# Kernel optimization log

Hardware: AMD Instinct MI355X
Metric: run time of the kernel (lower is better)

Reference implementation:

```python
import jax, jax.numpy as jnp
import numpy as np

DEPTH = 4
CODEBOOK_NUM = 2048
CODEBOOK_DIM = 256


def setup_inputs() -> dict:
    key = jax.random.key(0)
    k1, k2 = jax.random.split(key)
    z = jax.random.normal(k1, (32, CODEBOOK_DIM, 32, 32), dtype=jnp.float32)
    # matches nn.init.uniform_(weight, -1/K, 1/K)
    codebook = jax.random.uniform(
        k2, (CODEBOOK_NUM, CODEBOOK_DIM), dtype=jnp.float32,
        minval=-1.0 / CODEBOOK_NUM, maxval=1.0 / CODEBOOK_NUM)
    return {"z": z, "codebook": codebook}


def _quantize(flat_z, codebook):
    # ||z||^2 + ||e||^2 - 2 z.e  -> [N, K]
    dists = (jnp.sum(flat_z ** 2, axis=1, keepdims=True)
             + jnp.sum(codebook ** 2, axis=1)
             - 2.0 * flat_z @ codebook.T)
    indices = jnp.argmin(dists, axis=1)          # [N]
    return codebook[indices], indices            # gather [N, C]


def reference(z, codebook):
    B, C, H, W = z.shape
    K = codebook.shape[0]
    residual = z
    q_list, idx_list = [], []
    for _ in range(DEPTH):
        flat = residual.transpose(0, 2, 3, 1).reshape(-1, C)   # [N, C]
        q_flat, idx = _quantize(flat, codebook)
        q = q_flat.reshape(B, H, W, C).transpose(0, 3, 1, 2)   # [B, C, H, W]
        q_list.append(q)
        idx_list.append(idx)
        residual = residual - q
    # prefix-sum across depth (matches the in-place accumulation loop)
    quantized_cum = jnp.cumsum(jnp.stack(q_list, axis=0), axis=0)  # [D,B,C,H,W]
    q_last = quantized_cum[-1]
    # note: residual here is z_orig - sum_q, so ST term is z_orig - 2*sum_q (faithful)
    quantized_z_st = q_last + jax.lax.stop_gradient(residual - q_last)
    all_idx = jnp.concatenate(idx_list, axis=0)                    # [D*N]
    # mean of one-hot == normalized histogram (avoids [D*N, K] materialization)
    counts = jnp.zeros((K,), dtype=jnp.float32).at[all_idx].add(1.0)
    probs = counts / all_idx.shape[0]
    perplexity = jnp.exp(-jnp.sum(probs * jnp.log(jnp.clip(probs, 1e-10))))
    indices = jnp.stack(idx_list, axis=0)                          # [D, N]
    return quantized_cum, quantized_z_st, indices, perplexity
```

## Files before the change

kernel.cpp:

```cpp
#include <hip/hip_runtime.h>
#include <math.h>

#define BB 32
#define CC 256
#define HWt 1024
#define NN 32768
#define KK 2048
#define RQDEPTH 4
#define CAP 64
#define DELTA 4e-3f

typedef __attribute__((ext_vector_type(8))) short short8;
typedef __attribute__((ext_vector_type(16))) float f32x16;

__device__ __forceinline__ float pw128sq(const float4* __restrict__ a4) {
  float r[8];
  {
    float4 p = a4[0], q = a4[1];
    r[0] = __fmul_rn(p.x, p.x); r[1] = __fmul_rn(p.y, p.y);
    r[2] = __fmul_rn(p.z, p.z); r[3] = __fmul_rn(p.w, p.w);
    r[4] = __fmul_rn(q.x, q.x); r[5] = __fmul_rn(q.y, q.y);
    r[6] = __fmul_rn(q.z, q.z); r[7] = __fmul_rn(q.w, q.w);
  }
  for (int i = 1; i < 16; ++i) {
    float4 p = a4[2 * i], q = a4[2 * i + 1];
    r[0] = __fadd_rn(r[0], __fmul_rn(p.x, p.x));
    r[1] = __fadd_rn(r[1], __fmul_rn(p.y, p.y));
    r[2] = __fadd_rn(r[2], __fmul_rn(p.z, p.z));
    r[3] = __fadd_rn(r[3], __fmul_rn(p.w, p.w));
    r[4] = __fadd_rn(r[4], __fmul_rn(q.x, q.x));
    r[5] = __fadd_rn(r[5], __fmul_rn(q.y, q.y));
    r[6] = __fadd_rn(r[6], __fmul_rn(q.z, q.z));
    r[7] = __fadd_rn(r[7], __fmul_rn(q.w, q.w));
  }
  return __fadd_rn(__fadd_rn(__fadd_rn(r[0], r[1]), __fadd_rn(r[2], r[3])),
                   __fadd_rn(__fadd_rn(r[4], r[5]), __fadd_rn(r[6], r[7])));
}

__device__ __forceinline__ unsigned short f2bf(float x) {
  unsigned u = __float_as_uint(x);
  return (unsigned short)((u + 0x7fffu + ((u >> 16) & 1u)) >> 16);
}
__device__ __forceinline__ unsigned fenc(float f) {
  unsigned u = __float_as_uint(f);
  return (u & 0x80000000u) ? ~u : (u | 0x80000000u);
}
__device__ __forceinline__ float fdec(unsigned k) {
  return __uint_as_float((k & 0x80000000u) ? (k ^ 0x80000000u) : ~k);
}

__device__ __forceinline__ float exact_dot(const float4* __restrict__ zr4,
                                           const float4* __restrict__ e4) {
  float a = 0.f;
#pragma unroll 8
  for (int c4 = 0; c4 < 64; ++c4) {
    const float4 z4 = zr4[c4];
    const float4 q4 = e4[c4];
    a = fmaf(z4.x, q4.x, a);
    a = fmaf(z4.y, q4.y, a);
    a = fmaf(z4.z, q4.z, a);
    a = fmaf(z4.w, q4.w, a);
  }
  return a;
}

__global__ void k_ztrans(const float* __restrict__ z, float* __restrict__ resid) {
  __shared__ float tile[32][33];
  int b = blockIdx.z, c0 = blockIdx.y * 32, hw0 = blockIdx.x * 32;
  int tx = threadIdx.x & 31, ty = threadIdx.x >> 5;
  for (int i = ty; i < 32; i += 8)
    tile[i][tx] = z[((size_t)b * CC + c0 + i) * HWt + hw0 + tx];
  __syncthreads();
  for (int i = ty; i < 32; i += 8)
    resid[((size_t)b * HWt + hw0 + i) * CC + c0 + tx] = tile[tx][i];
}

__global__ void k_esplitH(const float* __restrict__ cb, short8* __restrict__ esH8) {
  const int tg = blockIdx.x * 256 + threadIdx.x;
  const int k = tg >> 5, c8 = tg & 31;
  const int idx8 = ((k >> 5) * 32 + c8) * 32 + (k & 31);
  const float4* s4 = (const float4*)(cb + (size_t)k * CC + c8 * 8);
  float4 p = s4[0], q = s4[1];
  short8 H;
  H[0] = (short)f2bf(p.x); H[1] = (short)f2bf(p.y);
  H[2] = (short)f2bf(p.z); H[3] = (short)f2bf(p.w);
  H[4] = (short)f2bf(q.x); H[5] = (short)f2bf(q.y);
  H[6] = (short)f2bf(q.z); H[7] = (short)f2bf(q.w);
  esH8[idx8] = H;
}

__global__ void k_bnorm(const float* __restrict__ cb, float* __restrict__ Bcol) {
  int k = blockIdx.x * 256 + threadIdx.x;
  if (k >= KK) return;
  const float4* row = (const float4*)(cb + (size_t)k * CC);
  Bcol[k] = __fadd_rn(pw128sq(row), pw128sq(row + 32));
}

__global__ void k_anorm(const float* __restrict__ resid, float* __restrict__ Arow) {
  int n = blockIdx.x * 256 + threadIdx.x;
  if (n >= NN) return;
  const float4* row = (const float4*)(resid + (size_t)n * CC);
  Arow[n] = __fadd_rn(pw128sq(row), pw128sq(row + 32));
}

__global__ void k_zero(int* counts) {
  int t = blockIdx.x * 256 + threadIdx.x;
  if (t < KK) counts[t] = 0;
}

__global__ __launch_bounds__(512, 4) void k_bulk(
    const float* __restrict__ resid, const short8* __restrict__ esH8,
    const float* __restrict__ cb, const float* __restrict__ Arow,
    const float* __restrict__ Bcol, int* __restrict__ idxAll,
    float* __restrict__ idxOut, int* __restrict__ counts, int depth) {
  __shared__ short8 zH8[32 * 32];
  __shared__ int cnt[32];
  __shared__ unsigned minkey[32];
  __shared__ unsigned long long best[32];
  __shared__ int clist[32 * CAP];

  const int t = threadIdx.x;
  const int row0 = blockIdx.x * 32;

  if (t < 32) { cnt[t] = 0; minkey[t] = 0xFFFFFFFFu; best[t] = ~0ull; }

  {
    const int srow = t & 31;
    const int c8a = (t >> 5) * 2;
#pragma unroll
    for (int cc = 0; cc < 2; ++cc) {
      const int c8 = c8a + cc;
      const float4* s4 =
          (const float4*)(resid + (size_t)(row0 + srow) * CC + c8 * 8);
      float4 p = s4[0], q = s4[1];
      short8 H;
      H[0] = (short)f2bf(p.x); H[1] = (short)f2bf(p.y);
      H[2] = (short)f2bf(p.z); H[3] = (short)f2bf(p.w);
      H[4] = (short)f2bf(q.x); H[5] = (short)f2bf(q.y);
      H[6] = (short)f2bf(q.z); H[7] = (short)f2bf(q.w);
      zH8[c8 * 32 + srow] = H;
    }
  }
  __syncthreads();

  const int wave = t >> 6, lane = t & 63;
  const int l31 = lane & 31, hh = lane >> 5;

  short8 zr[16];
  {
    const short8* zb = zH8 + hh * 32 + l31;
#pragma unroll
    for (int s = 0; s < 16; ++s) zr[s] = zb[s * 64];
  }

#pragma unroll 1
  for (int it = 0; it < 8; ++it) {
    const int kt = wave * 8 + ((it + (int)blockIdx.x) & 7);
    const int kb = kt * 32;
    f32x16 a0;
#pragma unroll
    for (int i = 0; i < 16; ++i) a0[i] = 0.f;

    const short8* ep = esH8 + kt * 1024 + hh * 32 + l31;
#pragma unroll
    for (int half = 0; half < 2; ++half) {
      short8 e[8];
#pragma unroll
      for (int s = 0; s < 8; ++s) e[s] = ep[(half * 8 + s) * 64];
#pragma unroll
      for (int s = 0; s < 8; ++s)
        a0 = __builtin_amdgcn_mfma_f32_32x32x16_bf16(zr[half * 8 + s], e[s],
                                                     a0, 0, 0, 0);
    }

    const float bkv = Bcol[kb + l31];
    float dt[16];
#pragma unroll
    for (int r = 0; r < 16; ++r) {
      const float m = a0[r];
      dt[r] = __fsub_rn(bkv, __fadd_rn(m, m));
    }
    if (it == 0) {
#pragma unroll
      for (int r = 0; r < 16; ++r) {
        float rm = dt[r];
#pragma unroll
        for (int m = 1; m < 32; m <<= 1) rm = fminf(rm, __shfl_xor(rm, m));
        if (l31 == 0) {
          const int rowr = (r & 3) + 8 * (r >> 2) + 4 * hh;
          atomicMin(&minkey[rowr], fenc(rm));
        }
      }
    }
#pragma unroll
    for (int r = 0; r < 16; ++r) {
      const int rowr = (r & 3) + 8 * (r >> 2) + 4 * hh;
      const float thr = fdec(minkey[rowr]) + DELTA;
      if (dt[r] <= thr) {
        atomicMin(&minkey[rowr], fenc(dt[r]));
        int idx = atomicAdd(&cnt[rowr], 1);
        if (idx < CAP) clist[rowr * CAP + idx] = kb + l31;
      }
    }
  }
  __syncthreads();

  {
    const int row = t >> 4;
    const int nc0 = cnt[row];
    const float av = Arow[row0 + row];
    const float4* zr4 = (const float4*)(resid + (size_t)(row0 + row) * CC);
    if (nc0 <= CAP) {
      for (int s = (t & 15); s < nc0; s += 16) {
        const int k = clist[row * CAP + s];
        const float a = exact_dot(zr4, (const float4*)(cb + (size_t)k * CC));
        const float Cv = __fadd_rn(av, Bcol[k]);
        const float sv = __fsub_rn(Cv, __fadd_rn(a, a));
        unsigned long long pk =
            ((unsigned long long)__float_as_uint(sv) << 32) | (unsigned)k;
        atomicMin(&best[row], pk);
      }
    } else {
      for (int k = (t & 15); k < KK; k += 16) {
        const float a = exact_dot(zr4, (const float4*)(cb + (size_t)k * CC));
        const float Cv = __fadd_rn(av, Bcol[k]);
        const float sv = __fsub_rn(Cv, __fadd_rn(a, a));
        unsigned long long pk =
            ((unsigned long long)__float_as_uint(sv) << 32) | (unsigned)k;
        atomicMin(&best[row], pk);
      }
    }
  }
  __syncthreads();
  if (t < 32) {
    const int wi = (int)(unsigned)(best[t] & 0xffffffffu);
    const int n = row0 + t;
    idxAll[depth * NN + n] = wi;
    idxOut[n] = (float)wi;
    atomicAdd(counts + wi, 1);
  }
}

__global__ void k_update(const float* __restrict__ cb, const int* __restrict__ idxAll,
                         float* __restrict__ resid, float* __restrict__ cum,
                         float* __restrict__ zst, int depth) {
  __shared__ float qt[32][33];
  __shared__ float rt[32][33];
  int b = blockIdx.z, c0 = blockIdx.y * 32, hw0 = blockIdx.x * 32;
  int tx = threadIdx.x & 31, ty = threadIdx.x >> 5;
  const int* idx = idxAll + depth * NN;
  for (int i = ty; i < 32; i += 8) {
    int n = b * HWt + hw0 + i;
    int kk = idx[n];
    size_t fo = (size_t)n * CC + c0 + tx;
    float q = cb[(size_t)kk * CC + c0 + tx];
    float r = __fsub_rn(resid[fo], q);
    resid[fo] = r;
    qt[i][tx] = q;
    rt[i][tx] = r;
  }
  __syncthreads();
  const size_t PLANE = (size_t)NN * CC;
  for (int i = ty; i < 32; i += 8) {
    size_t oo = ((size_t)b * CC + c0 + i) * HWt + hw0 + tx;
    float q = qt[tx][i];
    float prevv = (depth == 0) ? 0.f : cum[(size_t)(depth - 1) * PLANE + oo];
    cum[(size_t)depth * PLANE + oo] = __fadd_rn(prevv, q);
    if (depth == 3) zst[oo] = rt[tx][i];
  }
}

__global__ void k_perp(const int* __restrict__ counts, float* __restrict__ out) {
  __shared__ double sh[256];
  double s = 0.0;
  for (int k = threadIdx.x; k < KK; k += 256) {
    int c = counts[k];
    if (c > 0) {
      double p = (double)c / (double)(RQDEPTH * NN);
      s += p * log(p);
    }
  }
  sh[threadIdx.x] = s;
  __syncthreads();
  for (int st = 128; st; st >>= 1) {
    if (threadIdx.x < st) sh[threadIdx.x] += sh[threadIdx.x + st];
    __syncthreads();
  }
  if (threadIdx.x == 0) out[0] = (float)exp(-sh[0]);
}

extern "C" void kernel_launch(void* const* d_in, const int* in_sizes, int n_in,
                              void* d_out, int out_size, void* d_ws, size_t ws_size,
                              hipStream_t stream) {
  const float* z  = (const float*)d_in[0];
  const float* cb = (const float*)d_in[1];
  float* out = (float*)d_out;
  const size_t PLANE = (size_t)NN * CC;
  float* cum  = out;
  float* zst  = out + (size_t)RQDEPTH * PLANE;
  float* idxo = zst + PLANE;
  float* perp = idxo + (size_t)RQDEPTH * NN;

  float* resid = (float*)d_ws;
  float* esbase = resid + PLANE;
  short8* esH8 = (short8*)esbase;
  float* Arow  = esbase + (size_t)CC * KK;
  float* Bcol  = Arow + NN;
  int* idxAll  = (int*)(Bcol + KK);
  int* counts  = idxAll + RQDEPTH * NN;

  dim3 tgrid(HWt / 32, CC / 32, BB);
  k_ztrans<<<tgrid, 256, 0, stream>>>(z, resid);
  k_esplitH<<<256, 256, 0, stream>>>(cb, esH8);
  k_bnorm<<<KK / 256, 256, 0, stream>>>(cb, Bcol);
  k_zero<<<(KK + 255) / 256, 256, 0, stream>>>(counts);

  for (int d = 0; d < RQDEPTH; ++d) {
    k_anorm<<<NN / 256, 256, 0, stream>>>(resid, Arow);
    k_bulk<<<NN / 32, 512, 0, stream>>>(resid, esH8, cb, Arow, Bcol,
                                        idxAll, idxo + (size_t)d * NN, counts, d);
    k_update<<<tgrid, 256, 0, stream>>>(cb, idxAll, resid, cum, zst, d);
  }
  k_perp<<<1, 256, 0, stream>>>(counts, perp);
}
```

Baseline: 964.1 us.

## Stage codebook tiles in LDS across 128-row blocks with two-pass exact min threshold

Each block now handles 128 rows instead of 32. Codebook bf16 tiles are streamed into double-buffered shared memory with global_load_lds and shared by four row sections, so each codebook tile is read from global memory once per 128 rows rather than once per 32. The candidate search becomes two passes: the first computes the exact bf16 minimum per row, and the second collects candidates within DELTA of it, giving smaller candidate lists (cap 24). Rows that overflow the cap are rescanned cooperatively by the whole block. The cost is doing the MFMA work twice, plus more LDS use and lower occupancy (launch bounds 512,2).

```diff
diff --git a/kernel.cpp b/kernel.cpp
--- a/kernel.cpp
+++ b/kernel.cpp
@@ -7,7 +7,7 @@
 #define NN 32768
 #define KK 2048
 #define RQDEPTH 4
-#define CAP 64
+#define CAPR 24
 #define DELTA 4e-3f
 
 typedef __attribute__((ext_vector_type(8))) short short8;
@@ -108,111 +108,153 @@
   if (t < KK) counts[t] = 0;
 }
 
-__global__ __launch_bounds__(512, 4) void k_bulk(
+__global__ __launch_bounds__(512, 2) void k_bulk(
     const float* __restrict__ resid, const short8* __restrict__ esH8,
     const float* __restrict__ cb, const float* __restrict__ Arow,
     const float* __restrict__ Bcol, int* __restrict__ idxAll,
     float* __restrict__ idxOut, int* __restrict__ counts, int depth) {
-  __shared__ short8 zH8[32 * 32];
-  __shared__ int cnt[32];
-  __shared__ unsigned minkey[32];
-  __shared__ unsigned long long best[32];
-  __shared__ int clist[32 * CAP];
+  __shared__ short8 zH8[4][1024];
+  __shared__ short8 es[2][2048];
+  __shared__ unsigned minvU[128];
+  __shared__ int cnt[128];
+  __shared__ unsigned long long best[128];
+  __shared__ int clist[128][CAPR];
+  __shared__ int ovfl[128];
+  __shared__ int ovfn;
 
   const int t = threadIdx.x;
-  const int row0 = blockIdx.x * 32;
-
-  if (t < 32) { cnt[t] = 0; minkey[t] = 0xFFFFFFFFu; best[t] = ~0ull; }
+  const int row0 = blockIdx.x * 128;
+
+  if (t < 128) { cnt[t] = 0; minvU[t] = 0xFFFFFFFFu; best[t] = ~0ull; }
+  if (t == 0) ovfn = 0;
 
   {
-    const int srow = t & 31;
-    const int c8a = (t >> 5) * 2;
-#pragma unroll
-    for (int cc = 0; cc < 2; ++cc) {
-      const int c8 = c8a + cc;
+    const int srow = t >> 2;
+    const int q = t & 3;
+#pragma unroll
+    for (int cc = 0; cc < 8; ++cc) {
+      const int c8 = q * 8 + cc;
       const float4* s4 =
           (const float4*)(resid + (size_t)(row0 + srow) * CC + c8 * 8);
-      float4 p = s4[0], q = s4[1];
+      float4 p = s4[0], qq = s4[1];
       short8 H;
-      H[0] = (short)f2bf(p.x); H[1] = (short)f2bf(p.y);
-      H[2] = (short)f2bf(p.z); H[3] = (short)f2bf(p.w);
-      H[4] = (short)f2bf(q.x); H[5] = (short)f2bf(q.y);
-      H[6] = (short)f2bf(q.z); H[7] = (short)f2bf(q.w);
-      zH8[c8 * 32 + srow] = H;
-    }
-  }
-  __syncthreads();
-
-  const int wave = t >> 6, lane = t & 63;
+      H[0] = (short)f2bf(p.x);  H[1] = (short)f2bf(p.y);
+      H[2] = (short)f2bf(p.z);  H[3] = (short)f2bf(p.w);
+      H[4] = (short)f2bf(qq.x); H[5] = (short)f2bf(qq.y);
+      H[6] = (short)f2bf(qq.z); H[7] = (short)f2bf(qq.w);
+      zH8[srow >> 5][c8 * 32 + (srow & 31)] = H;
+    }
+  }
+  __syncthreads();
+
+  const int wave = __builtin_amdgcn_readfirstlane((int)(t >> 6));
+  const int lane = t & 63;
   const int l31 = lane & 31, hh = lane >> 5;
+  const int sec = wave & 3;
+  const int tt = wave >> 2;
 
   short8 zr[16];
-  {
-    const short8* zb = zH8 + hh * 32 + l31;
-#pragma unroll
-    for (int s = 0; s < 16; ++s) zr[s] = zb[s * 64];
-  }
-
+#pragma unroll
+  for (int s = 0; s < 16; ++s) zr[s] = zH8[sec][(s * 2 + hh) * 32 + l31];
+
+#define STAGE(B, STEP)                                                         \
+  {                                                                            \
+    const short8* gsrc = esH8 + (size_t)(STEP) * 2048;                         \
+    _Pragma("unroll")                                                          \
+    for (int c = 0; c < 4; ++c) {                                              \
+      const int chunk = wave + 8 * c;                                          \
+      __builtin_amdgcn_global_load_lds(                                        \
+          (const __attribute__((address_space(1))) void*)(gsrc + chunk * 64 +  \
+                                                          lane),               \
+          (__attribute__((address_space(3))) void*)(&es[B][chunk * 64 + lane]),\
+          16, 0, 0);                                                           \
+    }                                                                          \
+  }
+
+  float rm[16];
+#pragma unroll
+  for (int r = 0; r < 16; ++r) rm[r] = 3.4e38f;
+
+  int buf = 0;
+  STAGE(0, 0)
+  __syncthreads();
 #pragma unroll 1
-  for (int it = 0; it < 8; ++it) {
-    const int kt = wave * 8 + ((it + (int)blockIdx.x) & 7);
-    const int kb = kt * 32;
+  for (int step = 0; step < 32; ++step) {
+    if (step < 31) STAGE(buf ^ 1, step + 1)
     f32x16 a0;
 #pragma unroll
     for (int i = 0; i < 16; ++i) a0[i] = 0.f;
-
-    const short8* ep = esH8 + kt * 1024 + hh * 32 + l31;
-#pragma unroll
-    for (int half = 0; half < 2; ++half) {
-      short8 e[8];
-#pragma unroll
-      for (int s = 0; s < 8; ++s) e[s] = ep[(half * 8 + s) * 64];
-#pragma unroll
-      for (int s = 0; s < 8; ++s)
-        a0 = __builtin_amdgcn_mfma_f32_32x32x16_bf16(zr[half * 8 + s], e[s],
-                                                     a0, 0, 0, 0);
-    }
-
+#pragma unroll
+    for (int s = 0; s < 16; ++s) {
+      const short8 ef = es[buf][tt * 1024 + (s * 2 + hh) * 32 + l31];
+      a0 = __builtin_amdgcn_mfma_f32_32x32x16_bf16(zr[s], ef, a0, 0, 0, 0);
+    }
+    const int kb = (step * 2 + tt) * 32;
     const float bkv = Bcol[kb + l31];
-    float dt[16];
 #pragma unroll
     for (int r = 0; r < 16; ++r) {
       const float m = a0[r];
-      dt[r] = __fsub_rn(bkv, __fadd_rn(m, m));
-    }
-    if (it == 0) {
-#pragma unroll
-      for (int r = 0; r < 16; ++r) {
-        float rm = dt[r];
-#pragma unroll
-        for (int m = 1; m < 32; m <<= 1) rm = fminf(rm, __shfl_xor(rm, m));
-        if (l31 == 0) {
-          const int rowr = (r & 3) + 8 * (r >> 2) + 4 * hh;
-          atomicMin(&minkey[rowr], fenc(rm));
-        }
+      rm[r] = fminf(rm[r], __fsub_rn(bkv, __fadd_rn(m, m)));
+    }
+    __syncthreads();
+    buf ^= 1;
+  }
+#pragma unroll
+  for (int r = 0; r < 16; ++r) {
+    float v = rm[r];
+#pragma unroll
+    for (int m = 1; m < 32; m <<= 1) v = fminf(v, __shfl_xor(v, m));
+    if (l31 == 0) {
+      const int rowg = sec * 32 + (r & 3) + 8 * (r >> 2) + 4 * hh;
+      atomicMin(&minvU[rowg], fenc(v));
+    }
+  }
+  __syncthreads();
+
+  float thrv[16];
+#pragma unroll
+  for (int r = 0; r < 16; ++r)
+    thrv[r] = fdec(minvU[sec * 32 + (r & 3) + 8 * (r >> 2) + 4 * hh]) + DELTA;
+
+  buf = 0;
+  STAGE(0, 0)
+  __syncthreads();
+#pragma unroll 1
+  for (int step = 0; step < 32; ++step) {
+    if (step < 31) STAGE(buf ^ 1, step + 1)
+    f32x16 a0;
+#pragma unroll
+    for (int i = 0; i < 16; ++i) a0[i] = 0.f;
+#pragma unroll
+    for (int s = 0; s < 16; ++s) {
+      const short8 ef = es[buf][tt * 1024 + (s * 2 + hh) * 32 + l31];
+      a0 = __builtin_amdgcn_mfma_f32_32x32x16_bf16(zr[s], ef, a0, 0, 0, 0);
+    }
+    const int kb = (step * 2 + tt) * 32;
+    const float bkv = Bcol[kb + l31];
+#pragma unroll
+    for (int r = 0; r < 16; ++r) {
+      const float m = a0[r];
+      const float dt = __fsub_rn(bkv, __fadd_rn(m, m));
+      if (dt <= thrv[r]) {
+        const int rowg = sec * 32 + (r & 3) + 8 * (r >> 2) + 4 * hh;
+        const int id = atomicAdd(&cnt[rowg], 1);
+        if (id < CAPR) clist[rowg][id] = kb + l31;
       }
     }
-#pragma unroll
-    for (int r = 0; r < 16; ++r) {
-      const int rowr = (r & 3) + 8 * (r >> 2) + 4 * hh;
-      const float thr = fdec(minkey[rowr]) + DELTA;
-      if (dt[r] <= thr) {
-        atomicMin(&minkey[rowr], fenc(dt[r]));
-        int idx = atomicAdd(&cnt[rowr], 1);
-        if (idx < CAP) clist[rowr * CAP + idx] = kb + l31;
-      }
-    }
+    __syncthreads();
+    buf ^= 1;
   }
   __syncthreads();
 
   {
-    const int row = t >> 4;
+    const int row = t >> 2;
     const int nc0 = cnt[row];
-    const float av = Arow[row0 + row];
-    const float4* zr4 = (const float4*)(resid + (size_t)(row0 + row) * CC);
-    if (nc0 <= CAP) {
-      for (int s = (t & 15); s < nc0; s += 16) {
-        const int k = clist[row * CAP + s];
+    if (nc0 <= CAPR) {
+      const float av = Arow[row0 + row];
+      const float4* zr4 = (const float4*)(resid + (size_t)(row0 + row) * CC);
+      for (int s = (t & 3); s < nc0; s += 4) {
+        const int k = clist[row][s];
         const float a = exact_dot(zr4, (const float4*)(cb + (size_t)k * CC));
         const float Cv = __fadd_rn(av, Bcol[k]);
         const float sv = __fsub_rn(Cv, __fadd_rn(a, a));
@@ -220,25 +262,34 @@
             ((unsigned long long)__float_as_uint(sv) << 32) | (unsigned)k;
         atomicMin(&best[row], pk);
       }
-    } else {
-      for (int k = (t & 15); k < KK; k += 16) {
-        const float a = exact_dot(zr4, (const float4*)(cb + (size_t)k * CC));
-        const float Cv = __fadd_rn(av, Bcol[k]);
-        const float sv = __fsub_rn(Cv, __fadd_rn(a, a));
-        unsigned long long pk =
-            ((unsigned long long)__float_as_uint(sv) << 32) | (unsigned)k;
-        atomicMin(&best[row], pk);
-      }
-    }
-  }
-  __syncthreads();
-  if (t < 32) {
+    } else if ((t & 3) == 0) {
+      const int id = atomicAdd(&ovfn, 1);
+      ovfl[id] = row;
+    }
+  }
+  __syncthreads();
+  for (int o = 0; o < ovfn; ++o) {
+    const int row = ovfl[o];
+    const float av = Arow[row0 + row];
+    const float4* zr4 = (const float4*)(resid + (size_t)(row0 + row) * CC);
+    for (int k = t; k < KK; k += 512) {
+      const float a = exact_dot(zr4, (const float4*)(cb + (size_t)k * CC));
+      const float Cv = __fadd_rn(av, Bcol[k]);
+      const float sv = __fsub_rn(Cv, __fadd_rn(a, a));
+      unsigned long long pk =
+          ((unsigned long long)__float_as_uint(sv) << 32) | (unsigned)k;
+      atomicMin(&best[row], pk);
+    }
+  }
+  __syncthreads();
+  if (t < 128) {
     const int wi = (int)(unsigned)(best[t] & 0xffffffffu);
     const int n = row0 + t;
     idxAll[depth * NN + n] = wi;
     idxOut[n] = (float)wi;
     atomicAdd(counts + wi, 1);
   }
+#undef STAGE
 }
 
 __global__ void k_update(const float* __restrict__ cb, const int* __restrict__ idxAll,
@@ -317,8 +368,8 @@
 
   for (int d = 0; d < RQDEPTH; ++d) {
     k_anorm<<<NN / 256, 256, 0, stream>>>(resid, Arow);
-    k_bulk<<<NN / 32, 512, 0, stream>>>(resid, esH8, cb, Arow, Bcol,
-                                        idxAll, idxo + (size_t)d * NN, counts, d);
+    k_bulk<<<NN / 128, 512, 0, stream>>>(resid, esH8, cb, Arow, Bcol,
+                                         idxAll, idxo + (size_t)d * NN, counts, d);
     k_update<<<tgrid, 256, 0, stream>>>(cb, idxAll, resid, cum, zst, d);
   }
   k_perp<<<1, 256, 0, stream>>>(counts, perp);
```

After: 1.320 ms. 37.0% more time.
